# Optimization experiments

Hardware: AMD Instinct MI355X
Metric: run time of the kernel (lower is better)

## Reference

```python
import jax, jax.numpy as jnp
import numpy as np

B, S, DIM, H, FFN = 2, 2048, 1024, 16, 4096
HD = DIM // H
THETA = 10000.0
EPS = 1e-5


def setup_inputs() -> dict:
    key = jax.random.key(0)
    ks = jax.random.split(key, 12)
    s = 0.02
    return {
        "x": jax.random.normal(ks[0], (B, S, DIM), jnp.float32),
        "padding_mask": jnp.zeros((B, S), jnp.bool_),
        "qkv_w": jax.random.normal(ks[1], (DIM, 3 * DIM), jnp.float32) * s,
        "qkv_b": jnp.zeros((3 * DIM,), jnp.float32),
        "out_w": jax.random.normal(ks[2], (DIM, DIM), jnp.float32) * s,
        "out_b": jnp.zeros((DIM,), jnp.float32),
        "ln1_g": jnp.ones((DIM,), jnp.float32),
        "ln1_b": jnp.zeros((DIM,), jnp.float32),
        "ln2_g": jnp.ones((DIM,), jnp.float32),
        "ln2_b": jnp.zeros((DIM,), jnp.float32),
        "w1": jax.random.normal(ks[3], (DIM, FFN), jnp.float32) * s,
        "b1": jnp.zeros((FFN,), jnp.float32),
        "w2": jax.random.normal(ks[4], (FFN, DIM), jnp.float32) * s,
        "b2": jnp.zeros((DIM,), jnp.float32),
    }


def _layer_norm(x, g, b):
    mu = jnp.mean(x, axis=-1, keepdims=True)
    var = jnp.mean(jnp.square(x - mu), axis=-1, keepdims=True)
    return (x - mu) * jax.lax.rsqrt(var + EPS) * g + b


def _rotate_half(x):
    x1, x2 = jnp.split(x, 2, axis=-1)
    return jnp.concatenate([-x2, x1], axis=-1)


def reference(x, padding_mask, qkv_w, qkv_b, out_w, out_b,
              ln1_g, ln1_b, ln2_g, ln2_b, w1, b1, w2, b2):
    b, s, _ = x.shape
    residual = x
    h = _layer_norm(x, ln1_g, ln1_b)
    qkv = h @ qkv_w + qkv_b  # [b, s, 3*dim]
    q, k, v = jnp.split(qkv, 3, axis=-1)
    # [b, heads, s, head_dim]
    q = q.reshape(b, s, H, HD).transpose(0, 2, 1, 3)
    k = k.reshape(b, s, H, HD).transpose(0, 2, 1, 3)
    v = v.reshape(b, s, H, HD).transpose(0, 2, 1, 3)

    # rotary embeddings
    pos = jnp.arange(s, dtype=jnp.float32)
    inv_freq = 1.0 / (THETA ** (jnp.arange(0, HD, 2, dtype=jnp.float32) / HD))
    freqs = pos[:, None] * inv_freq[None, :]          # [s, hd/2]
    emb = jnp.concatenate([freqs, freqs], axis=-1)    # [s, hd]
    sin = jnp.sin(emb)[None, None, :, :]
    cos = jnp.cos(emb)[None, None, :, :]
    q = q * cos + _rotate_half(q) * sin
    k = k * cos + _rotate_half(k) * sin

    scale = HD ** (-0.5)
    scores = jnp.einsum('bhqd,bhkd->bhqk', q, k) * scale
    neg = jnp.finfo(scores.dtype).min
    scores = jnp.where(padding_mask[:, None, None, :], neg, scores)
    probs = jax.nn.softmax(scores, axis=-1)
    ctx = jnp.einsum('bhqk,bhkd->bhqd', probs, v)
    ctx = ctx.transpose(0, 2, 1, 3).reshape(b, s, DIM)
    x = residual + (ctx @ out_w + out_b)

    residual = x
    h = _layer_norm(x, ln2_g, ln2_b)
    h = jax.nn.gelu(h @ w1 + b1, approximate=False) @ w2 + b2
    return residual + h
```

## Files before the change

kernel.cpp:

```cpp
#include <hip/hip_runtime.h>
#include <hip/hip_bf16.h>
#include <math.h>

typedef __hip_bfloat16 bf16;
typedef __attribute__((ext_vector_type(8))) short short8;
typedef __attribute__((ext_vector_type(4))) float floatx4;

constexpr int BB   = 2;
constexpr int SS   = 2048;
constexpr int DIMc = 1024;
constexpr int Hc   = 16;
constexpr int HDc  = 64;
constexpr int FFNc = 4096;
constexpr int TOK  = BB * SS;
constexpr float EPSc = 1e-5f;

typedef __attribute__((address_space(1))) void gvoid;
typedef __attribute__((address_space(3))) void lvoid;
__device__ __forceinline__ void lds16(const void* g, void* l) {
    __builtin_amdgcn_global_load_lds((gvoid*)g, (lvoid*)l, 16, 0, 0);
}

__device__ __forceinline__ float fexp2(float x) { return __builtin_amdgcn_exp2f(x); }

__global__ __launch_bounds__(256) void ln_kernel(const float* __restrict__ x,
                                                 const float* __restrict__ g,
                                                 const float* __restrict__ b,
                                                 bf16* __restrict__ out) {
    int t = blockIdx.x;
    int tid = threadIdx.x;
    const float4* xr = (const float4*)(x + (size_t)t * DIMc);
    float4 v = xr[tid];
    float s  = v.x + v.y + v.z + v.w;
    float sq = v.x*v.x + v.y*v.y + v.z*v.z + v.w*v.w;
    for (int off = 1; off < 64; off <<= 1) {
        s  += __shfl_xor(s,  off, 64);
        sq += __shfl_xor(sq, off, 64);
    }
    __shared__ float ss[4], ssq[4];
    int wave = tid >> 6;
    if ((tid & 63) == 0) { ss[wave] = s; ssq[wave] = sq; }
    __syncthreads();
    s  = ss[0] + ss[1] + ss[2] + ss[3];
    sq = ssq[0] + ssq[1] + ssq[2] + ssq[3];
    float mu  = s * (1.0f / DIMc);
    float var = sq * (1.0f / DIMc) - mu * mu;
    float inv = rsqrtf(var + EPSc);
    float4 gg = ((const float4*)g)[tid];
    float4 bb = ((const float4*)b)[tid];
    size_t base = (size_t)t * DIMc + tid * 4;
    out[base + 0] = __float2bfloat16((v.x - mu) * inv * gg.x + bb.x);
    out[base + 1] = __float2bfloat16((v.y - mu) * inv * gg.y + bb.y);
    out[base + 2] = __float2bfloat16((v.z - mu) * inv * gg.z + bb.z);
    out[base + 3] = __float2bfloat16((v.w - mu) * inv * gg.w + bb.w);
}

__global__ __launch_bounds__(256) void transpose_bf16(const float* __restrict__ in,
                                                      bf16* __restrict__ out,
                                                      int K, int N) {
    __shared__ float t[32][33];
    int k0 = blockIdx.y * 32, n0 = blockIdx.x * 32;
    int x = threadIdx.x & 31;
    int y = threadIdx.x >> 5;
#pragma unroll
    for (int i = 0; i < 4; ++i) {
        int k = y + i * 8;
        t[k][x] = in[(size_t)(k0 + k) * N + n0 + x];
    }
    __syncthreads();
#pragma unroll
    for (int i = 0; i < 4; ++i) {
        int n = y + i * 8;
        out[(size_t)(n0 + n) * K + k0 + x] = __float2bfloat16(t[x][n]);
    }
}

template <int ACT, bool ADD_RES, bool OUT_BF16>
__global__ __launch_bounds__(256) void gemm_bt(const bf16* __restrict__ A,
                                               const bf16* __restrict__ Bt,
                                               const float* __restrict__ bias,
                                               const float* __restrict__ res,
                                               void* __restrict__ Cout,
                                               int M, int N, int K) {
    constexpr int BM = 128, BN = 128, BK = 32;
    __shared__ bf16 As[BM * BK];
    __shared__ bf16 Bs[BN * BK];
    const int tid = threadIdx.x;
    const int wave = tid >> 6, lane = tid & 63;
    const int lane15 = lane & 15, lgrp = lane >> 4;
    const int wm = (wave >> 1) * 64, wn = (wave & 1) * 64;
    const int row0 = blockIdx.y * BM, col0 = blockIdx.x * BN;

    floatx4 acc[4][4] = {};

    const int sr = tid >> 2;
    const int sc = (tid & 3) * 8;
    const bf16* ga = A  + (size_t)(row0 + sr) * K + sc;
    const bf16* gb = Bt + (size_t)(col0 + sr) * K + sc;
    bf16* la = As + wave * 512;
    bf16* lb = Bs + wave * 512;

    for (int k0 = 0; k0 < K; k0 += BK) {
        __syncthreads();
        lds16(ga + k0,                  la);
        lds16(ga + k0 + (size_t)64 * K, la + 2048);
        lds16(gb + k0,                  lb);
        lds16(gb + k0 + (size_t)64 * K, lb + 2048);
        __syncthreads();
        short8 af[4], bfr[4];
#pragma unroll
        for (int i = 0; i < 4; ++i)
            af[i] = *(const short8*)(As + (wm + i * 16 + lane15) * BK + lgrp * 8);
#pragma unroll
        for (int j = 0; j < 4; ++j)
            bfr[j] = *(const short8*)(Bs + (wn + j * 16 + lane15) * BK + lgrp * 8);
#pragma unroll
        for (int i = 0; i < 4; ++i)
#pragma unroll
            for (int j = 0; j < 4; ++j)
                acc[i][j] = __builtin_amdgcn_mfma_f32_16x16x32_bf16(af[i], bfr[j], acc[i][j], 0, 0, 0);
    }

#pragma unroll
    for (int i = 0; i < 4; ++i) {
#pragma unroll
        for (int j = 0; j < 4; ++j) {
            int col = col0 + wn + j * 16 + lane15;
            float bv = bias[col];
#pragma unroll
            for (int r = 0; r < 4; ++r) {
                int row = row0 + wm + i * 16 + lgrp * 4 + r;
                float v = acc[i][j][r] + bv;
                if (ACT == 1) v = 0.5f * v * (1.0f + erff(v * 0.70710678118654752f));
                if (ADD_RES) v += res[(size_t)row * N + col];
                if (OUT_BF16) ((bf16*)Cout)[(size_t)row * N + col] = __float2bfloat16(v);
                else          ((float*)Cout)[(size_t)row * N + col] = v;
            }
        }
    }
}

__global__ __launch_bounds__(256) void rope_kernel(bf16* __restrict__ qkv) {
    int t = blockIdx.x;
    int pos = t % SS;
    int tid = threadIdx.x;
    const float ln_theta = 9.210340371976184f;
    for (int idx = tid; idx < 1024; idx += 256) {
        int which = idx >> 9;
        int p = idx & 511;
        int head = p >> 5, d = p & 31;
        float inv_freq = __expf(-((float)(2 * d) / (float)HDc) * ln_theta);
        float ang = (float)pos * inv_freq;
        float sn, cs;
        __sincosf(ang, &sn, &cs);
        size_t base = (size_t)t * (3 * DIMc) + (size_t)which * DIMc + head * HDc + d;
        float x1 = __bfloat162float(qkv[base]);
        float x2 = __bfloat162float(qkv[base + 32]);
        qkv[base]      = __float2bfloat16(x1 * cs - x2 * sn);
        qkv[base + 32] = __float2bfloat16(x2 * cs + x1 * sn);
    }
}

__global__ __launch_bounds__(256) void attn_mfma(const bf16* __restrict__ qkv,
                                                 const unsigned char* __restrict__ mask,
                                                 bf16* __restrict__ ctx) {
    __shared__ short Klds[2][64][32];
    __shared__ short Vt[64][72];
    __shared__ short Ps[4][16][72];
    __shared__ float mkf[64];

    const int b = blockIdx.z, h = blockIdx.y, q0 = blockIdx.x * 64;
    const int tid = threadIdx.x;
    const int wave = tid >> 6, lane = tid & 63;
    const int lane15 = lane & 15, lgrp = lane >> 4;
    const short* qs = (const short*)qkv;

    short* qstage = &Ps[wave][0][0];
#pragma unroll
    for (int i = 0; i < 2; ++i) {
        int idx = i * 64 + lane;
        int g = idx & 3, row = (idx >> 2) & 15, s = idx >> 6;
        const short* gq = qs + (size_t)(b * SS + q0 + wave * 16 + row) * 3072
                             + h * 64 + s * 32 + g * 8;
        lds16(gq, qstage + i * 512);
    }
    __syncthreads();
    short8 aQ[2];
#pragma unroll
    for (int s = 0; s < 2; ++s)
        aQ[s] = *(const short8*)(qstage + s * 512 + lane15 * 32 + lgrp * 8);

    const short8 bOnes = (short8)(short)0x3F80;
    floatx4 O[4] = {};
    floatx4 Lacc = {};
    const float cscale = 0.18033688011112042f;

    for (int k0 = 0; k0 < SS; k0 += 64) {
        __syncthreads();
#pragma unroll
        for (int i = 0; i < 2; ++i) {
            int idx = wave * 128 + i * 64 + lane;
            int g = idx & 3, row = (idx >> 2) & 63, s = idx >> 8;
            const short* gk = qs + (size_t)(b * SS + k0 + row) * 3072 + 1024
                                 + h * 64 + s * 32 + g * 8;
            lds16(gk, &Klds[0][0][0] + (wave * 128 + i * 64) * 8);
        }
#pragma unroll
        for (int c = 0; c < 2; ++c) {
            int idx = c * 256 + tid;
            int dgrp = idx >> 6, kk = idx & 63;
            const short8 vv = *(const short8*)(qs + (size_t)(b * SS + k0 + kk) * 3072
                                               + 2048 + h * 64 + dgrp * 8);
#pragma unroll
            for (int j = 0; j < 8; ++j) Vt[dgrp * 8 + j][kk] = vv[j];
        }
        if (tid < 16) {
            const unsigned char* mp = mask + b * SS + k0 + tid * 4;
#pragma unroll
            for (int j = 0; j < 4; ++j) mkf[tid * 4 + j] = mp[j] ? -1e30f : 0.0f;
        }
        __syncthreads();

        short8 bK[4][2];
#pragma unroll
        for (int j = 0; j < 4; ++j)
#pragma unroll
            for (int s = 0; s < 2; ++s)
                bK[j][s] = *(const short8*)&Klds[s][j * 16 + lane15][lgrp * 8];
        floatx4 Sf[4] = {};
#pragma unroll
        for (int j = 0; j < 4; ++j)
#pragma unroll
            for (int s = 0; s < 2; ++s)
                Sf[j] = __builtin_amdgcn_mfma_f32_16x16x32_bf16(aQ[s], bK[j][s], Sf[j], 0, 0, 0);

        float mkv[4];
#pragma unroll
        for (int j = 0; j < 4; ++j) mkv[j] = mkf[j * 16 + lane15];

#pragma unroll
        for (int r = 0; r < 4; ++r) {
#pragma unroll
            for (int j = 0; j < 4; ++j) {
                float p = fexp2(Sf[j][r] * cscale + mkv[j]);
                bf16 t = __float2bfloat16(p);
                Ps[wave][lgrp * 4 + r][lane15 + 16 * j] = *(short*)&t;
            }
        }

        short8 aP[2], bV[4][2];
#pragma unroll
        for (int s = 0; s < 2; ++s)
            aP[s] = *(const short8*)&Ps[wave][lane15][s * 32 + lgrp * 8];
#pragma unroll
        for (int jd = 0; jd < 4; ++jd)
#pragma unroll
            for (int s = 0; s < 2; ++s)
                bV[jd][s] = *(const short8*)&Vt[jd * 16 + lane15][s * 32 + lgrp * 8];
#pragma unroll
        for (int jd = 0; jd < 4; ++jd)
#pragma unroll
            for (int s = 0; s < 2; ++s)
                O[jd] = __builtin_amdgcn_mfma_f32_16x16x32_bf16(aP[s], bV[jd][s], O[jd], 0, 0, 0);
#pragma unroll
        for (int s = 0; s < 2; ++s)
            Lacc = __builtin_amdgcn_mfma_f32_16x16x32_bf16(aP[s], bOnes, Lacc, 0, 0, 0);
    }

#pragma unroll
    for (int r = 0; r < 4; ++r) {
        float inv = 1.0f / Lacc[r];
        size_t rowoff = (size_t)(b * SS + q0 + wave * 16 + lgrp * 4 + r) * DIMc
                        + h * 64 + lane15;
#pragma unroll
        for (int jd = 0; jd < 4; ++jd)
            ctx[rowoff + jd * 16] = __float2bfloat16(O[jd][r] * inv);
    }
}

extern "C" void kernel_launch(void* const* d_in, const int* in_sizes, int n_in,
                              void* d_out, int out_size, void* d_ws, size_t ws_size,
                              hipStream_t stream) {
    const float* x      = (const float*)d_in[0];
    const unsigned char* pmask = (const unsigned char*)d_in[1];
    const float* qkv_w  = (const float*)d_in[2];
    const float* qkv_b  = (const float*)d_in[3];
    const float* out_w  = (const float*)d_in[4];
    const float* out_b  = (const float*)d_in[5];
    const float* ln1_g  = (const float*)d_in[6];
    const float* ln1_b  = (const float*)d_in[7];
    const float* ln2_g  = (const float*)d_in[8];
    const float* ln2_b  = (const float*)d_in[9];
    const float* w1     = (const float*)d_in[10];
    const float* b1     = (const float*)d_in[11];
    const float* w2     = (const float*)d_in[12];
    const float* b2     = (const float*)d_in[13];
    float* out = (float*)d_out;

    char* ws = (char*)d_ws;
    bf16* wqkv_t = (bf16*)ws;                      ws += (size_t)3072 * 1024 * 2;
    bf16* wout_t = (bf16*)ws;                      ws += (size_t)1024 * 1024 * 2;
    bf16* w1_t   = (bf16*)ws;                      ws += (size_t)4096 * 1024 * 2;
    bf16* w2_t   = (bf16*)ws;                      ws += (size_t)1024 * 4096 * 2;
    bf16* h_bf   = (bf16*)ws;                      ws += (size_t)TOK * DIMc * 2;
    bf16* qkv_bf = (bf16*)ws;                      ws += (size_t)TOK * 3 * DIMc * 2;
    bf16* ctx_bf = (bf16*)ws;                      ws += (size_t)TOK * DIMc * 2;
    bf16* ffn1_bf = qkv_bf;

    transpose_bf16<<<dim3(3072 / 32, 1024 / 32), 256, 0, stream>>>(qkv_w, wqkv_t, 1024, 3072);
    transpose_bf16<<<dim3(1024 / 32, 1024 / 32), 256, 0, stream>>>(out_w, wout_t, 1024, 1024);
    transpose_bf16<<<dim3(4096 / 32, 1024 / 32), 256, 0, stream>>>(w1,    w1_t,   1024, 4096);
    transpose_bf16<<<dim3(1024 / 32, 4096 / 32), 256, 0, stream>>>(w2,    w2_t,   4096, 1024);

    ln_kernel<<<TOK, 256, 0, stream>>>(x, ln1_g, ln1_b, h_bf);
    gemm_bt<0, false, true><<<dim3(3072 / 128, TOK / 128), 256, 0, stream>>>(
        h_bf, wqkv_t, qkv_b, nullptr, qkv_bf, TOK, 3 * DIMc, DIMc);
    rope_kernel<<<TOK, 256, 0, stream>>>(qkv_bf);
    attn_mfma<<<dim3(SS / 64, Hc, BB), 256, 0, stream>>>(qkv_bf, pmask, ctx_bf);
    gemm_bt<0, true, false><<<dim3(1024 / 128, TOK / 128), 256, 0, stream>>>(
        ctx_bf, wout_t, out_b, x, out, TOK, DIMc, DIMc);
    ln_kernel<<<TOK, 256, 0, stream>>>(out, ln2_g, ln2_b, h_bf);
    gemm_bt<1, false, true><<<dim3(4096 / 128, TOK / 128), 256, 0, stream>>>(
        h_bf, w1_t, b1, nullptr, ffn1_bf, TOK, FFNc, DIMc);
    gemm_bt<0, true, false><<<dim3(1024 / 128, TOK / 128), 256, 0, stream>>>(
        ffn1_bf, w2_t, b2, out, out, TOK, DIMc, FFNc);
}
```

Before: 450.0 us.

## Split-K atomic GEMMs for narrow outputs and 32-row-per-wave attention tiles

Adds a split-K GEMM that accumulates partial products into the fp32 output with atomicAdd. It is used for the output projection (2 chunks) and the FFN down projection (4 chunks), with the residual pre-copied into the output for the first, so these N=1024 GEMMs launch more blocks. Separately, the attention kernel now gives each wave two 16-row query tiles, so each block covers 128 queries and every K/V tile loaded into LDS is reused twice as much. The trade-offs are atomic traffic, an extra device copy, nondeterministic summation order, and higher register pressure in attention with half as many attention blocks.

```diff
diff --git a/kernel.cpp b/kernel.cpp
--- a/kernel.cpp
+++ b/kernel.cpp
@@ -135,6 +135,67 @@
                 if (ADD_RES) v += res[(size_t)row * N + col];
                 if (OUT_BF16) ((bf16*)Cout)[(size_t)row * N + col] = __float2bfloat16(v);
                 else          ((float*)Cout)[(size_t)row * N + col] = v;
+            }
+        }
+    }
+}
+
+__global__ __launch_bounds__(256) void gemm_bt_atomic(const bf16* __restrict__ A,
+                                                      const bf16* __restrict__ Bt,
+                                                      const float* __restrict__ bias,
+                                                      float* __restrict__ Cout,
+                                                      int M, int N, int K, int KCH) {
+    constexpr int BM = 128, BN = 128, BK = 32;
+    __shared__ bf16 As[BM * BK];
+    __shared__ bf16 Bs[BN * BK];
+    const int tid = threadIdx.x;
+    const int wave = tid >> 6, lane = tid & 63;
+    const int lane15 = lane & 15, lgrp = lane >> 4;
+    const int wm = (wave >> 1) * 64, wn = (wave & 1) * 64;
+    const int row0 = blockIdx.y * BM, col0 = blockIdx.x * BN;
+    const int kbase = blockIdx.z * KCH;
+
+    floatx4 acc[4][4] = {};
+
+    const int sr = tid >> 2;
+    const int sc = (tid & 3) * 8;
+    const bf16* ga = A  + (size_t)(row0 + sr) * K + sc;
+    const bf16* gb = Bt + (size_t)(col0 + sr) * K + sc;
+    bf16* la = As + wave * 512;
+    bf16* lb = Bs + wave * 512;
+
+    for (int k0 = kbase; k0 < kbase + KCH; k0 += BK) {
+        __syncthreads();
+        lds16(ga + k0,                  la);
+        lds16(ga + k0 + (size_t)64 * K, la + 2048);
+        lds16(gb + k0,                  lb);
+        lds16(gb + k0 + (size_t)64 * K, lb + 2048);
+        __syncthreads();
+        short8 af[4], bfr[4];
+#pragma unroll
+        for (int i = 0; i < 4; ++i)
+            af[i] = *(const short8*)(As + (wm + i * 16 + lane15) * BK + lgrp * 8);
+#pragma unroll
+        for (int j = 0; j < 4; ++j)
+            bfr[j] = *(const short8*)(Bs + (wn + j * 16 + lane15) * BK + lgrp * 8);
+#pragma unroll
+        for (int i = 0; i < 4; ++i)
+#pragma unroll
+            for (int j = 0; j < 4; ++j)
+                acc[i][j] = __builtin_amdgcn_mfma_f32_16x16x32_bf16(af[i], bfr[j], acc[i][j], 0, 0, 0);
+    }
+
+    const bool addb = (blockIdx.z == 0);
+#pragma unroll
+    for (int i = 0; i < 4; ++i) {
+#pragma unroll
+        for (int j = 0; j < 4; ++j) {
+            int col = col0 + wn + j * 16 + lane15;
+            float bv = addb ? bias[col] : 0.0f;
+#pragma unroll
+            for (int r = 0; r < 4; ++r) {
+                int row = row0 + wm + i * 16 + lgrp * 4 + r;
+                atomicAdd(&Cout[(size_t)row * N + col], acc[i][j][r] + bv);
             }
         }
     }
@@ -166,10 +227,10 @@
                                                  bf16* __restrict__ ctx) {
     __shared__ short Klds[2][64][32];
     __shared__ short Vt[64][72];
-    __shared__ short Ps[4][16][72];
+    __shared__ short Ps[4][32][72];
     __shared__ float mkf[64];
 
-    const int b = blockIdx.z, h = blockIdx.y, q0 = blockIdx.x * 64;
+    const int b = blockIdx.z, h = blockIdx.y, q0 = blockIdx.x * 128;
     const int tid = threadIdx.x;
     const int wave = tid >> 6, lane = tid & 63;
     const int lane15 = lane & 15, lgrp = lane >> 4;
@@ -177,22 +238,24 @@
 
     short* qstage = &Ps[wave][0][0];
 #pragma unroll
-    for (int i = 0; i < 2; ++i) {
+    for (int i = 0; i < 4; ++i) {
         int idx = i * 64 + lane;
-        int g = idx & 3, row = (idx >> 2) & 15, s = idx >> 6;
-        const short* gq = qs + (size_t)(b * SS + q0 + wave * 16 + row) * 3072
+        int g = idx & 3, row = (idx >> 2) & 15, s = (idx >> 6) & 1, mi = idx >> 7;
+        const short* gq = qs + (size_t)(b * SS + q0 + wave * 32 + mi * 16 + row) * 3072
                              + h * 64 + s * 32 + g * 8;
-        lds16(gq, qstage + i * 512);
+        lds16(gq, qstage + idx * 8);
     }
     __syncthreads();
-    short8 aQ[2];
-#pragma unroll
-    for (int s = 0; s < 2; ++s)
-        aQ[s] = *(const short8*)(qstage + s * 512 + lane15 * 32 + lgrp * 8);
+    short8 aQ[2][2];
+#pragma unroll
+    for (int mi = 0; mi < 2; ++mi)
+#pragma unroll
+        for (int s = 0; s < 2; ++s)
+            aQ[mi][s] = *(const short8*)(qstage + ((mi * 2 + s) * 16 + lane15) * 32 + lgrp * 8);
 
     const short8 bOnes = (short8)(short)0x3F80;
-    floatx4 O[4] = {};
-    floatx4 Lacc = {};
+    floatx4 O[2][4] = {};
+    floatx4 Lacc[2] = {};
     const float cscale = 0.18033688011112042f;
 
     for (int k0 = 0; k0 < SS; k0 += 64) {
@@ -203,7 +266,7 @@
             int g = idx & 3, row = (idx >> 2) & 63, s = idx >> 8;
             const short* gk = qs + (size_t)(b * SS + k0 + row) * 3072 + 1024
                                  + h * 64 + s * 32 + g * 8;
-            lds16(gk, &Klds[0][0][0] + (wave * 128 + i * 64) * 8);
+            lds16(gk, &Klds[0][0][0] + idx * 8);
         }
 #pragma unroll
         for (int c = 0; c < 2; ++c) {
@@ -227,55 +290,65 @@
 #pragma unroll
             for (int s = 0; s < 2; ++s)
                 bK[j][s] = *(const short8*)&Klds[s][j * 16 + lane15][lgrp * 8];
-        floatx4 Sf[4] = {};
-#pragma unroll
-        for (int j = 0; j < 4; ++j)
+        floatx4 Sf[2][4] = {};
+#pragma unroll
+        for (int mi = 0; mi < 2; ++mi)
+#pragma unroll
+            for (int j = 0; j < 4; ++j)
+#pragma unroll
+                for (int s = 0; s < 2; ++s)
+                    Sf[mi][j] = __builtin_amdgcn_mfma_f32_16x16x32_bf16(aQ[mi][s], bK[j][s], Sf[mi][j], 0, 0, 0);
+
+        float mkv[4];
+#pragma unroll
+        for (int j = 0; j < 4; ++j) mkv[j] = mkf[j * 16 + lane15];
+
+#pragma unroll
+        for (int mi = 0; mi < 2; ++mi)
+#pragma unroll
+            for (int r = 0; r < 4; ++r)
+#pragma unroll
+                for (int j = 0; j < 4; ++j) {
+                    float p = fexp2(Sf[mi][j][r] * cscale + mkv[j]);
+                    bf16 t = __float2bfloat16(p);
+                    Ps[wave][mi * 16 + lgrp * 4 + r][lane15 + 16 * j] = *(short*)&t;
+                }
+
+        short8 aP[2][2], bV[4][2];
+#pragma unroll
+        for (int mi = 0; mi < 2; ++mi)
 #pragma unroll
             for (int s = 0; s < 2; ++s)
-                Sf[j] = __builtin_amdgcn_mfma_f32_16x16x32_bf16(aQ[s], bK[j][s], Sf[j], 0, 0, 0);
-
-        float mkv[4];
-#pragma unroll
-        for (int j = 0; j < 4; ++j) mkv[j] = mkf[j * 16 + lane15];
-
-#pragma unroll
-        for (int r = 0; r < 4; ++r) {
-#pragma unroll
-            for (int j = 0; j < 4; ++j) {
-                float p = fexp2(Sf[j][r] * cscale + mkv[j]);
-                bf16 t = __float2bfloat16(p);
-                Ps[wave][lgrp * 4 + r][lane15 + 16 * j] = *(short*)&t;
-            }
-        }
-
-        short8 aP[2], bV[4][2];
-#pragma unroll
-        for (int s = 0; s < 2; ++s)
-            aP[s] = *(const short8*)&Ps[wave][lane15][s * 32 + lgrp * 8];
+                aP[mi][s] = *(const short8*)&Ps[wave][mi * 16 + lane15][s * 32 + lgrp * 8];
 #pragma unroll
         for (int jd = 0; jd < 4; ++jd)
 #pragma unroll
             for (int s = 0; s < 2; ++s)
                 bV[jd][s] = *(const short8*)&Vt[jd * 16 + lane15][s * 32 + lgrp * 8];
 #pragma unroll
-        for (int jd = 0; jd < 4; ++jd)
+        for (int mi = 0; mi < 2; ++mi) {
+#pragma unroll
+            for (int jd = 0; jd < 4; ++jd)
+#pragma unroll
+                for (int s = 0; s < 2; ++s)
+                    O[mi][jd] = __builtin_amdgcn_mfma_f32_16x16x32_bf16(aP[mi][s], bV[jd][s], O[mi][jd], 0, 0, 0);
 #pragma unroll
             for (int s = 0; s < 2; ++s)
-                O[jd] = __builtin_amdgcn_mfma_f32_16x16x32_bf16(aP[s], bV[jd][s], O[jd], 0, 0, 0);
-#pragma unroll
-        for (int s = 0; s < 2; ++s)
-            Lacc = __builtin_amdgcn_mfma_f32_16x16x32_bf16(aP[s], bOnes, Lacc, 0, 0, 0);
-    }
-
-#pragma unroll
-    for (int r = 0; r < 4; ++r) {
-        float inv = 1.0f / Lacc[r];
-        size_t rowoff = (size_t)(b * SS + q0 + wave * 16 + lgrp * 4 + r) * DIMc
-                        + h * 64 + lane15;
-#pragma unroll
-        for (int jd = 0; jd < 4; ++jd)
-            ctx[rowoff + jd * 16] = __float2bfloat16(O[jd][r] * inv);
-    }
+                Lacc[mi] = __builtin_amdgcn_mfma_f32_16x16x32_bf16(aP[mi][s], bOnes, Lacc[mi], 0, 0, 0);
+        }
+    }
+
+#pragma unroll
+    for (int mi = 0; mi < 2; ++mi)
+#pragma unroll
+        for (int r = 0; r < 4; ++r) {
+            float inv = 1.0f / Lacc[mi][r];
+            size_t rowoff = (size_t)(b * SS + q0 + wave * 32 + mi * 16 + lgrp * 4 + r) * DIMc
+                            + h * 64 + lane15;
+#pragma unroll
+            for (int jd = 0; jd < 4; ++jd)
+                ctx[rowoff + jd * 16] = __float2bfloat16(O[mi][jd][r] * inv);
+        }
 }
 
 extern "C" void kernel_launch(void* const* d_in, const int* in_sizes, int n_in,
@@ -316,12 +389,16 @@
     gemm_bt<0, false, true><<<dim3(3072 / 128, TOK / 128), 256, 0, stream>>>(
         h_bf, wqkv_t, qkv_b, nullptr, qkv_bf, TOK, 3 * DIMc, DIMc);
     rope_kernel<<<TOK, 256, 0, stream>>>(qkv_bf);
-    attn_mfma<<<dim3(SS / 64, Hc, BB), 256, 0, stream>>>(qkv_bf, pmask, ctx_bf);
-    gemm_bt<0, true, false><<<dim3(1024 / 128, TOK / 128), 256, 0, stream>>>(
-        ctx_bf, wout_t, out_b, x, out, TOK, DIMc, DIMc);
+    attn_mfma<<<dim3(SS / 128, Hc, BB), 256, 0, stream>>>(qkv_bf, pmask, ctx_bf);
+
+    hipMemcpyAsync(out, x, (size_t)TOK * DIMc * sizeof(float),
+                   hipMemcpyDeviceToDevice, stream);
+    gemm_bt_atomic<<<dim3(1024 / 128, TOK / 128, 2), 256, 0, stream>>>(
+        ctx_bf, wout_t, out_b, out, TOK, DIMc, DIMc, 512);
+
     ln_kernel<<<TOK, 256, 0, stream>>>(out, ln2_g, ln2_b, h_bf);
     gemm_bt<1, false, true><<<dim3(4096 / 128, TOK / 128), 256, 0, stream>>>(
         h_bf, w1_t, b1, nullptr, ffn1_bf, TOK, FFNc, DIMc);
-    gemm_bt<0, true, false><<<dim3(1024 / 128, TOK / 128), 256, 0, stream>>>(
-        ffn1_bf, w2_t, b2, out, out, TOK, DIMc, FFNc);
-}
+    gemm_bt_atomic<<<dim3(1024 / 128, TOK / 128, 4), 256, 0, stream>>>(
+        ffn1_bf, w2_t, b2, out, TOK, DIMc, FFNc, 1024);
+}
```

New measurement: 472.7 us. +5.1%, slower.
